# Optimization experiments

Hardware: AMD Instinct MI355X
Metric: run time of the kernel (lower is better)

## Reference

```python
import jax, jax.numpy as jnp
import numpy as np

B, T, DE, DD, A, FN, FS = 32, 2000, 512, 1024, 128, 32, 16
TEMPERATURE = 1.0


def setup_inputs() -> dict:
    key = jax.random.key(0)
    ks = jax.random.split(key, 10)
    input_enc = jax.random.normal(ks[0], (B, T, DE), dtype=jnp.float32)
    # lengths in [T//2, T] so no zero-length utterances
    enc_lengths = jax.random.randint(ks[1], (B,), T // 2, T + 1, dtype=jnp.int32)
    input_dec = jax.random.normal(ks[2], (B, DD), dtype=jnp.float32)
    # prev_att: previous-step attention weights (masked, normalized)
    prev_att = jax.random.uniform(ks[3], (B, T), dtype=jnp.float32)
    pad = jnp.arange(T)[None, :] >= enc_lengths[:, None]
    prev_att = jnp.where(pad, 0.0, prev_att)
    prev_att = prev_att / jnp.sum(prev_att, axis=1, keepdims=True)
    # parameters
    conv_w = jax.random.normal(ks[4], (FN, 1, 2 * FS + 1), dtype=jnp.float32) * 0.1  # [out,in,k]
    enc_w = jax.random.normal(ks[5], (A, DE), dtype=jnp.float32) * 0.04
    dec_w = jax.random.normal(ks[6], (A, DD), dtype=jnp.float32) * 0.03
    att_w = jax.random.normal(ks[7], (A, FN), dtype=jnp.float32) * 0.17
    att_b = jnp.zeros((A,), dtype=jnp.float32)
    out_w = jax.random.normal(ks[8], (1, A), dtype=jnp.float32) * 0.09
    return dict(input_enc=input_enc, enc_lengths=enc_lengths, input_dec=input_dec,
                prev_att=prev_att, conv_w=conv_w, enc_w=enc_w, dec_w=dec_w,
                att_w=att_w, att_b=att_b, out_w=out_w)


def reference(input_enc, enc_lengths, input_dec, prev_att,
              conv_w, enc_w, dec_w, att_w, att_b, out_w):
    b, t, _ = input_enc.shape
    fs = (conv_w.shape[-1] - 1) // 2  # 'same' padding
    # padding mask: True at padded positions t >= length
    mask = jnp.arange(t)[None, :] >= enc_lengths[:, None]  # [B,T]
    # location features: Conv1d over prev attention, 1 -> FN channels, same length
    conv = jax.lax.conv_general_dilated(
        prev_att[:, None, :], conv_w, window_strides=(1,),
        padding=[(fs, fs)], dimension_numbers=("NCH", "OIH", "NCH"))  # [B,FN,T]
    loc_feat = conv.transpose(0, 2, 1)  # [B,T,FN]
    projected_att = loc_feat @ att_w.T + att_b        # [B,T,A]
    projected_enc = input_enc @ enc_w.T               # [B,T,A]
    projected_dec = (input_dec @ dec_w.T)[:, None, :]  # [B,1,A]
    score = jnp.squeeze(jnp.tanh(projected_att + projected_enc + projected_dec) @ out_w.T, -1)  # [B,T]
    score = jnp.where(mask, -jnp.inf, score)
    att_weight = jax.nn.softmax(TEMPERATURE * score, axis=1)  # [B,T]
    context = jnp.einsum("btd,bt->bd", input_enc, att_weight)  # [B,DE]
    return context, att_weight
```

## Files before the change

kernel.cpp:

```cpp
#include <hip/hip_runtime.h>
#include <hip/hip_bf16.h>
#include <math.h>

#define B_ 32
#define T_ 2000
#define DE_ 512
#define DD_ 1024
#define A_ 128
#define FN_ 32
#define FS_ 16
#define KW_ (2*FS_+1)

typedef __bf16 bf16x8 __attribute__((ext_vector_type(8)));
typedef __bf16 bf16x4 __attribute__((ext_vector_type(4)));
typedef float f32x4 __attribute__((ext_vector_type(4)));

#define BT 64
#define LSTR 40

__device__ __forceinline__ void load_lds16(const void* g, void* l) {
    __builtin_amdgcn_global_load_lds(
        (const __attribute__((address_space(1))) unsigned int*)g,
        (__attribute__((address_space(3))) unsigned int*)l, 16, 0, 0);
}

__device__ __forceinline__ bf16x8 cvt8(float4 x, float4 y) {
    bf16x8 o;
    o[0] = (__bf16)x.x; o[1] = (__bf16)x.y; o[2] = (__bf16)x.z; o[3] = (__bf16)x.w;
    o[4] = (__bf16)y.x; o[5] = (__bf16)y.y; o[6] = (__bf16)y.z; o[7] = (__bf16)y.w;
    return o;
}

__global__ __launch_bounds__(256) void prep_kernel(
    const float* __restrict__ enc_w, const float* __restrict__ att_w,
    const float* __restrict__ input_dec, const float* __restrict__ dec_w,
    const float* __restrict__ att_b,
    __bf16* __restrict__ enc_bf, __bf16* __restrict__ att_bf,
    float* __restrict__ pdec, float* __restrict__ ctx_un )
{
    int bx = blockIdx.x, tid = threadIdx.x;
    if (bx < 64) {
        int i = bx * 256 + tid;
        float4 v = ((const float4*)enc_w)[i];
        bf16x4 o;
        o[0] = (__bf16)v.x; o[1] = (__bf16)v.y; o[2] = (__bf16)v.z; o[3] = (__bf16)v.w;
        *(bf16x4*)(enc_bf + (size_t)i * 4) = o;
        if (i < (A_ * FN_) / 4) {
            float4 w = ((const float4*)att_w)[i];
            bf16x4 p;
            p[0] = (__bf16)w.x; p[1] = (__bf16)w.y; p[2] = (__bf16)w.z; p[3] = (__bf16)w.w;
            *(bf16x4*)(att_bf + (size_t)i * 4) = p;
        }
    } else if (bx < 192) {
        int pb = bx - 64;
        int b  = pb >> 2;
        int a0 = (pb & 3) * 32;
        int al = tid >> 3;
        int kg = tid & 7;
        int a  = a0 + al;
        const float4* w = (const float4*)(dec_w + (size_t)a * DD_);
        const float4* x = (const float4*)(input_dec + (size_t)b * DD_);
        float acc = 0.f;
        #pragma unroll 8
        for (int j = 0; j < 32; j++) {
            int i4 = kg + j * 8;
            float4 wv = w[i4], xv = x[i4];
            acc += wv.x * xv.x + wv.y * xv.y + wv.z * xv.z + wv.w * xv.w;
        }
        acc += __shfl_xor(acc, 1, 64);
        acc += __shfl_xor(acc, 2, 64);
        acc += __shfl_xor(acc, 4, 64);
        if (kg == 0) pdec[b * A_ + a] = acc + att_b[a];
    } else {
        int idx = (bx - 192) * 256 + tid;
        if (idx < (B_ * DE_ + B_) / 4 + 1)
            ((float4*)ctx_un)[idx] = make_float4(0.f, 0.f, 0.f, 0.f);
    }
}

__global__ __launch_bounds__(256, 4) void score_kernel(
    const float* __restrict__ input_enc, const __bf16* __restrict__ enc_bf,
    const float* __restrict__ prev_att,  const float* __restrict__ conv_w,
    const __bf16* __restrict__ att_bf,   const float* __restrict__ pdec,
    const float* __restrict__ out_w,     const int* __restrict__ lengths,
    float* __restrict__ wbuf, float* __restrict__ ctx_un,
    float* __restrict__ denom)
{
    __shared__ __align__(16) char Bt[2][16384];
    __shared__ __align__(16) float pa_s[BT + 2 * FS_];
    __shared__ __align__(16) __bf16 loc_s[BT * LSTR];
    __shared__ float w_s[BT];

    const int tid = threadIdx.x;
    const int b  = blockIdx.y;
    const int t0 = blockIdx.x * BT;
    const int len = lengths[b];

    const int f    = tid & 31;
    const int rblk = tid >> 5;
    float cwr[KW_];
    #pragma unroll
    for (int k = 0; k < KW_; k++) cwr[k] = conv_w[f * KW_ + k];

    for (int j = tid; j < BT + 2 * FS_; j += 256) {
        int t = t0 - FS_ + j;
        pa_s[j] = (t >= 0 && t < T_) ? prev_att[b * T_ + t] : 0.f;
    }
    __syncthreads();

    {
        float par[40];
        #pragma unroll
        for (int j = 0; j < 10; j++)
            *(float4*)&par[j * 4] = *(const float4*)&pa_s[rblk * 8 + j * 4];
        float accv[8] = {0.f, 0.f, 0.f, 0.f, 0.f, 0.f, 0.f, 0.f};
        #pragma unroll
        for (int k = 0; k < KW_; k++) {
            float c = cwr[k];
            #pragma unroll
            for (int j = 0; j < 8; j++) accv[j] += par[j + k] * c;
        }
        #pragma unroll
        for (int j = 0; j < 8; j++)
            loc_s[(rblk * 8 + j) * LSTR + f] = (__bf16)accv[j];
    }
    __syncthreads();

    const int lane = tid & 63;
    const int wv   = tid >> 6;
    const int col  = lane & 15;
    const int grp  = lane >> 4;
    const int rowb = wv * 16 + col;
    const int t_row = t0 + rowb;
    const int t_clamp = t_row < T_ ? t_row : T_ - 1;
    const int sw = (col & 7);

    const float* arow = input_enc + ((size_t)(b * T_ + t_clamp)) * DE_ + grp * 8;

    bf16x8 afA[8];
    #pragma unroll
    for (int j = 0; j < 4; j++) {
        float4 r0 = *(const float4*)(arow + j * 64);
        float4 r1 = *(const float4*)(arow + j * 64 + 4);
        float4 r2 = *(const float4*)(arow + j * 64 + 32);
        float4 r3 = *(const float4*)(arow + j * 64 + 36);
        afA[2 * j]     = cvt8(r0, r1);
        afA[2 * j + 1] = cvt8(r2, r3);
    }

    f32x4 acc[8];
    const f32x4 zero = (f32x4){0.f, 0.f, 0.f, 0.f};

    {
        bf16x8 afrag = *(const bf16x8*)(loc_s + rowb * LSTR + grp * 8);
        #pragma unroll
        for (int i = 0; i < 8; i++) {
            bf16x8 bfrag = *(const bf16x8*)(att_bf + (size_t)(i * 16 + col) * FN_ + grp * 8);
            acc[i] = __builtin_amdgcn_mfma_f32_16x16x32_bf16(afrag, bfrag, zero, 0, 0, 0);
        }
    }

    bf16x8 afB[8];
    #pragma unroll
    for (int j = 0; j < 4; j++) {
        float4 r0 = *(const float4*)(arow + 256 + j * 64);
        float4 r1 = *(const float4*)(arow + 256 + j * 64 + 4);
        float4 r2 = *(const float4*)(arow + 256 + j * 64 + 32);
        float4 r3 = *(const float4*)(arow + 256 + j * 64 + 36);
        afB[2 * j]     = cvt8(r0, r1);
        afB[2 * j + 1] = cvt8(r2, r3);
    }

    #pragma unroll
    for (int j = 0; j < 4; j++) {
        int s  = j * 256 + tid;
        int r  = s >> 3;
        int cp = s & 7;
        int c  = cp ^ (r & 7);
        load_lds16(enc_bf + (size_t)r * DE_ + c * 8,
                   Bt[0] + j * 4096 + wv * 1024);
    }
    __syncthreads();

    int cur = 0;
    #pragma unroll
    for (int it = 0; it < 8; ++it) {
        const int kc = it * 64;
        if (it < 7) {
            #pragma unroll
            for (int j = 0; j < 4; j++) {
                int s  = j * 256 + tid;
                int r  = s >> 3;
                int cp = s & 7;
                int c  = cp ^ (r & 7);
                load_lds16(enc_bf + (size_t)r * DE_ + (kc + 64) + c * 8,
                           Bt[cur ^ 1] + j * 4096 + wv * 1024);
            }
        }

        bf16x8 af0, af1;
        if (it < 4) { af0 = afA[2 * it];       af1 = afA[2 * it + 1]; }
        else        { af0 = afB[2 * (it - 4)]; af1 = afB[2 * (it - 4) + 1]; }

        #pragma unroll
        for (int i = 0; i < 8; i++) {
            bf16x8 bfrag = *(const bf16x8*)(Bt[cur] + (i * 16 + col) * 128 + ((grp ^ sw) * 16));
            acc[i] = __builtin_amdgcn_mfma_f32_16x16x32_bf16(af0, bfrag, acc[i], 0, 0, 0);
        }
        #pragma unroll
        for (int i = 0; i < 8; i++) {
            bf16x8 bfrag = *(const bf16x8*)(Bt[cur] + (i * 16 + col) * 128 + (((4 + grp) ^ sw) * 16));
            acc[i] = __builtin_amdgcn_mfma_f32_16x16x32_bf16(af1, bfrag, acc[i], 0, 0, 0);
        }

        __syncthreads();
        cur ^= 1;
    }

    float s[4] = {0.f, 0.f, 0.f, 0.f};
    float Mabs = 0.f;
    #pragma unroll
    for (int i = 0; i < 8; i++) {
        int a = i * 16 + col;
        float ow = out_w[a];
        Mabs += fabsf(ow);
        float bias = pdec[b * A_ + a];
        #pragma unroll
        for (int r = 0; r < 4; r++) {
            float v = acc[i][r] + bias;
            v = fminf(fmaxf(v, -15.f), 15.f);
            float e = __expf(2.f * v);
            s[r] += ow * ((e - 1.f) / (e + 1.f));
        }
    }
    #pragma unroll
    for (int r = 0; r < 4; r++) {
        s[r] += __shfl_xor(s[r], 1, 64);
        s[r] += __shfl_xor(s[r], 2, 64);
        s[r] += __shfl_xor(s[r], 4, 64);
        s[r] += __shfl_xor(s[r], 8, 64);
    }
    Mabs += __shfl_xor(Mabs, 1, 64);
    Mabs += __shfl_xor(Mabs, 2, 64);
    Mabs += __shfl_xor(Mabs, 4, 64);
    Mabs += __shfl_xor(Mabs, 8, 64);

    if (col == 0) {
        #pragma unroll
        for (int r = 0; r < 4; r++) {
            int rl = wv * 16 + grp * 4 + r;
            int t = t0 + rl;
            float w = 0.f;
            if (t < len) w = __expf(s[r] - Mabs);
            w_s[rl] = w;
            if (t < T_) wbuf[b * T_ + t] = w;
        }
    }
    __syncthreads();

    if (tid < 64) {
        float w = w_s[tid];
        w += __shfl_xor(w, 1, 64);
        w += __shfl_xor(w, 2, 64);
        w += __shfl_xor(w, 4, 64);
        w += __shfl_xor(w, 8, 64);
        w += __shfl_xor(w, 16, 64);
        w += __shfl_xor(w, 32, 64);
        if (tid == 0) atomicAdd(&denom[b], w);
    }

    int n_eff = len - t0;
    if (n_eff > BT) n_eff = BT;
    if (n_eff > 0) {
        int d0 = tid * 2;
        const float* ebase = input_enc + ((size_t)(b * T_ + t0)) * DE_ + d0;
        float cx = 0.f, cy = 0.f;
        #pragma unroll 8
        for (int t = 0; t < n_eff; t++) {
            float w = w_s[t];
            float2 v = *(const float2*)(ebase + (size_t)t * DE_);
            cx += w * v.x;
            cy += w * v.y;
        }
        atomicAdd(&ctx_un[b * DE_ + d0 + 0], cx);
        atomicAdd(&ctx_un[b * DE_ + d0 + 1], cy);
    }
}

__global__ __launch_bounds__(256) void finalize_kernel(
    const float* __restrict__ wbuf, const float* __restrict__ ctx_un,
    const float* __restrict__ denom, float* __restrict__ out)
{
    int bx = blockIdx.x, tid = threadIdx.x;
    if (bx < 64) {
        int i4 = bx * 256 + tid;
        if (i4 < (B_ * T_) / 4) {
            int b = i4 / (T_ / 4);
            float inv = 1.f / denom[b];
            float4 w = ((const float4*)wbuf)[i4];
            w.x *= inv; w.y *= inv; w.z *= inv; w.w *= inv;
            ((float4*)(out + B_ * DE_))[i4] = w;
        }
    } else {
        int j = (bx - 64) * 256 + tid;
        int b = j / (DE_ / 4);
        float inv = 1.f / denom[b];
        float4 c = ((const float4*)ctx_un)[j];
        c.x *= inv; c.y *= inv; c.z *= inv; c.w *= inv;
        ((float4*)out)[j] = c;
    }
}

extern "C" void kernel_launch(void* const* d_in, const int* in_sizes, int n_in,
                              void* d_out, int out_size, void* d_ws, size_t ws_size,
                              hipStream_t stream)
{
    const float* input_enc   = (const float*)d_in[0];
    const int*   enc_lengths = (const int*)d_in[1];
    const float* input_dec   = (const float*)d_in[2];
    const float* prev_att    = (const float*)d_in[3];
    const float* conv_w      = (const float*)d_in[4];
    const float* enc_w       = (const float*)d_in[5];
    const float* dec_w       = (const float*)d_in[6];
    const float* att_w       = (const float*)d_in[7];
    const float* att_b       = (const float*)d_in[8];
    const float* out_w       = (const float*)d_in[9];

    float* out = (float*)d_out;
    char* ws = (char*)d_ws;
    float*  pdec   = (float*)ws;
    float*  wbuf   = (float*)(ws + 16384);
    __bf16* enc_bf = (__bf16*)(ws + 272384);
    __bf16* att_bf = (__bf16*)(ws + 403456);
    float*  ctx_un = (float*)(ws + 411648);
    float*  denom  = (float*)(ws + 477184);

    prep_kernel<<<209, 256, 0, stream>>>(enc_w, att_w, input_dec, dec_w, att_b,
                                         enc_bf, att_bf, pdec, ctx_un);

    dim3 sgrid((T_ + BT - 1) / BT, B_);
    score_kernel<<<sgrid, 256, 0, stream>>>(input_enc, enc_bf, prev_att, conv_w,
                                            att_bf, pdec, out_w, enc_lengths,
                                            wbuf, ctx_un, denom);

    finalize_kernel<<<80, 256, 0, stream>>>(wbuf, ctx_un, denom, out);
}
```

Baseline: 234.3 us.

## Enlarge score tile to 256 rows and keep full encoder weight resident in LDS

The score kernel now uses 1024-thread blocks covering 256 time steps instead of 64. The whole bf16 encoder projection weight is loaded into LDS once at kernel start, replacing the double-buffered per-chunk streaming and its per-iteration barriers. Input rows are loaded and converted inside the k-loop instead of being preloaded into registers, and the context accumulation is split across four row groups. This amortizes weight loads over more rows and removes in-loop syncs, at the cost of roughly 150KB of LDS per block, one block per CU, and load latency now exposed inside the MFMA loop.

Result: slower. 240.6 us (+2.7%).

```diff
diff --git a/kernel.cpp b/kernel.cpp
--- a/kernel.cpp
+++ b/kernel.cpp
@@ -15,7 +15,7 @@
 typedef __bf16 bf16x4 __attribute__((ext_vector_type(4)));
 typedef float f32x4 __attribute__((ext_vector_type(4)));
 
-#define BT 64
+#define BT 256
 #define LSTR 40
 
 __device__ __forceinline__ void load_lds16(const void* g, void* l) {
@@ -78,7 +78,7 @@
     }
 }
 
-__global__ __launch_bounds__(256, 4) void score_kernel(
+__global__ __launch_bounds__(1024, 4) void score_kernel(
     const float* __restrict__ input_enc, const __bf16* __restrict__ enc_bf,
     const float* __restrict__ prev_att,  const float* __restrict__ conv_w,
     const __bf16* __restrict__ att_bf,   const float* __restrict__ pdec,
@@ -86,25 +86,37 @@
     float* __restrict__ wbuf, float* __restrict__ ctx_un,
     float* __restrict__ denom)
 {
-    __shared__ __align__(16) char Bt[2][16384];
+    __shared__ __align__(16) char Bt[8][16384];
     __shared__ __align__(16) float pa_s[BT + 2 * FS_];
     __shared__ __align__(16) __bf16 loc_s[BT * LSTR];
     __shared__ float w_s[BT];
 
-    const int tid = threadIdx.x;
+    const int tid  = threadIdx.x;
+    const int lane = tid & 63;
+    const int wv   = tid >> 6;
     const int b  = blockIdx.y;
     const int t0 = blockIdx.x * BT;
     const int len = lengths[b];
 
+    #pragma unroll
+    for (int j = 0; j < 8; j++) {
+        int w  = wv * 64 + lane;
+        int r  = w >> 3;
+        int cp = w & 7;
+        int c  = cp ^ (r & 7);
+        load_lds16(enc_bf + (size_t)r * DE_ + j * 64 + c * 8,
+                   Bt[j] + wv * 1024);
+    }
+
     const int f    = tid & 31;
     const int rblk = tid >> 5;
     float cwr[KW_];
     #pragma unroll
     for (int k = 0; k < KW_; k++) cwr[k] = conv_w[f * KW_ + k];
 
-    for (int j = tid; j < BT + 2 * FS_; j += 256) {
-        int t = t0 - FS_ + j;
-        pa_s[j] = (t >= 0 && t < T_) ? prev_att[b * T_ + t] : 0.f;
+    if (tid < BT + 2 * FS_) {
+        int t = t0 - FS_ + tid;
+        pa_s[tid] = (t >= 0 && t < T_) ? prev_att[b * T_ + t] : 0.f;
     }
     __syncthreads();
 
@@ -126,8 +138,6 @@
     }
     __syncthreads();
 
-    const int lane = tid & 63;
-    const int wv   = tid >> 6;
     const int col  = lane & 15;
     const int grp  = lane >> 4;
     const int rowb = wv * 16 + col;
@@ -135,19 +145,6 @@
     const int t_clamp = t_row < T_ ? t_row : T_ - 1;
     const int sw = (col & 7);
 
-    const float* arow = input_enc + ((size_t)(b * T_ + t_clamp)) * DE_ + grp * 8;
-
-    bf16x8 afA[8];
-    #pragma unroll
-    for (int j = 0; j < 4; j++) {
-        float4 r0 = *(const float4*)(arow + j * 64);
-        float4 r1 = *(const float4*)(arow + j * 64 + 4);
-        float4 r2 = *(const float4*)(arow + j * 64 + 32);
-        float4 r3 = *(const float4*)(arow + j * 64 + 36);
-        afA[2 * j]     = cvt8(r0, r1);
-        afA[2 * j + 1] = cvt8(r2, r3);
-    }
-
     f32x4 acc[8];
     const f32x4 zero = (f32x4){0.f, 0.f, 0.f, 0.f};
 
@@ -160,61 +157,28 @@
         }
     }
 
-    bf16x8 afB[8];
-    #pragma unroll
-    for (int j = 0; j < 4; j++) {
-        float4 r0 = *(const float4*)(arow + 256 + j * 64);
-        float4 r1 = *(const float4*)(arow + 256 + j * 64 + 4);
-        float4 r2 = *(const float4*)(arow + 256 + j * 64 + 32);
-        float4 r3 = *(const float4*)(arow + 256 + j * 64 + 36);
-        afB[2 * j]     = cvt8(r0, r1);
-        afB[2 * j + 1] = cvt8(r2, r3);
-    }
-
-    #pragma unroll
-    for (int j = 0; j < 4; j++) {
-        int s  = j * 256 + tid;
-        int r  = s >> 3;
-        int cp = s & 7;
-        int c  = cp ^ (r & 7);
-        load_lds16(enc_bf + (size_t)r * DE_ + c * 8,
-                   Bt[0] + j * 4096 + wv * 1024);
-    }
-    __syncthreads();
-
-    int cur = 0;
+    const float* arow = input_enc + ((size_t)(b * T_ + t_clamp)) * DE_ + grp * 8;
+
     #pragma unroll
     for (int it = 0; it < 8; ++it) {
         const int kc = it * 64;
-        if (it < 7) {
-            #pragma unroll
-            for (int j = 0; j < 4; j++) {
-                int s  = j * 256 + tid;
-                int r  = s >> 3;
-                int cp = s & 7;
-                int c  = cp ^ (r & 7);
-                load_lds16(enc_bf + (size_t)r * DE_ + (kc + 64) + c * 8,
-                           Bt[cur ^ 1] + j * 4096 + wv * 1024);
-            }
-        }
-
-        bf16x8 af0, af1;
-        if (it < 4) { af0 = afA[2 * it];       af1 = afA[2 * it + 1]; }
-        else        { af0 = afB[2 * (it - 4)]; af1 = afB[2 * (it - 4) + 1]; }
+        float4 r0 = *(const float4*)(arow + kc);
+        float4 r1 = *(const float4*)(arow + kc + 4);
+        float4 r2 = *(const float4*)(arow + kc + 32);
+        float4 r3 = *(const float4*)(arow + kc + 36);
+        bf16x8 af0 = cvt8(r0, r1);
+        bf16x8 af1 = cvt8(r2, r3);
 
         #pragma unroll
         for (int i = 0; i < 8; i++) {
-            bf16x8 bfrag = *(const bf16x8*)(Bt[cur] + (i * 16 + col) * 128 + ((grp ^ sw) * 16));
+            bf16x8 bfrag = *(const bf16x8*)(Bt[it] + (i * 16 + col) * 128 + ((grp ^ sw) * 16));
             acc[i] = __builtin_amdgcn_mfma_f32_16x16x32_bf16(af0, bfrag, acc[i], 0, 0, 0);
         }
         #pragma unroll
         for (int i = 0; i < 8; i++) {
-            bf16x8 bfrag = *(const bf16x8*)(Bt[cur] + (i * 16 + col) * 128 + (((4 + grp) ^ sw) * 16));
+            bf16x8 bfrag = *(const bf16x8*)(Bt[it] + (i * 16 + col) * 128 + (((4 + grp) ^ sw) * 16));
             acc[i] = __builtin_amdgcn_mfma_f32_16x16x32_bf16(af1, bfrag, acc[i], 0, 0, 0);
         }
-
-        __syncthreads();
-        cur ^= 1;
     }
 
     float s[4] = {0.f, 0.f, 0.f, 0.f};
@@ -259,7 +223,7 @@
     __syncthreads();
 
     if (tid < 64) {
-        float w = w_s[tid];
+        float w = w_s[tid] + w_s[tid + 64] + w_s[tid + 128] + w_s[tid + 192];
         w += __shfl_xor(w, 1, 64);
         w += __shfl_xor(w, 2, 64);
         w += __shfl_xor(w, 4, 64);
@@ -272,18 +236,23 @@
     int n_eff = len - t0;
     if (n_eff > BT) n_eff = BT;
     if (n_eff > 0) {
-        int d0 = tid * 2;
-        const float* ebase = input_enc + ((size_t)(b * T_ + t0)) * DE_ + d0;
-        float cx = 0.f, cy = 0.f;
-        #pragma unroll 8
-        for (int t = 0; t < n_eff; t++) {
-            float w = w_s[t];
-            float2 v = *(const float2*)(ebase + (size_t)t * DE_);
-            cx += w * v.x;
-            cy += w * v.y;
-        }
-        atomicAdd(&ctx_un[b * DE_ + d0 + 0], cx);
-        atomicAdd(&ctx_un[b * DE_ + d0 + 1], cy);
+        int rg  = tid >> 8;
+        int d0  = (tid & 255) * 2;
+        int rlo = rg * 64;
+        int rhi = rlo + 64 < n_eff ? rlo + 64 : n_eff;
+        if (rhi > rlo) {
+            const float* ebase = input_enc + ((size_t)(b * T_ + t0 + rlo)) * DE_ + d0;
+            float cx = 0.f, cy = 0.f;
+            #pragma unroll 8
+            for (int r = 0; r < rhi - rlo; r++) {
+                float w = w_s[rlo + r];
+                float2 v = *(const float2*)(ebase + (size_t)r * DE_);
+                cx += w * v.x;
+                cy += w * v.y;
+            }
+            atomicAdd(&ctx_un[b * DE_ + d0 + 0], cx);
+            atomicAdd(&ctx_un[b * DE_ + d0 + 1], cy);
+        }
     }
 }
 
@@ -339,9 +308,9 @@
                                          enc_bf, att_bf, pdec, ctx_un);
 
     dim3 sgrid((T_ + BT - 1) / BT, B_);
-    score_kernel<<<sgrid, 256, 0, stream>>>(input_enc, enc_bf, prev_att, conv_w,
-                                            att_bf, pdec, out_w, enc_lengths,
-                                            wbuf, ctx_un, denom);
+    score_kernel<<<sgrid, 1024, 0, stream>>>(input_enc, enc_bf, prev_att, conv_w,
+                                             att_bf, pdec, out_w, enc_lengths,
+                                             wbuf, ctx_un, denom);
 
     finalize_kernel<<<80, 256, 0, stream>>>(wbuf, ctx_un, denom, out);
 }
```
